# Performance work log

Measured on AMD Instinct MI355X. Metric: run time of the kernel, lower is better.

Reference implementation:

```python
import jax, jax.numpy as jnp
import numpy as np

B, C, H, W = 2, 14, 128, 128
LOSS_WEIGHT = 0.5  # output = (1 - loss_weight) * sum of per-(bs,cls) log-Hausdorff losses
BIG = 1e6          # 'infinite' 1D distance for columns with no background pixel


def _edt_sq(is_zero):
    """Exact squared Euclidean distance transform of a [H,W] bool map.

    Returns, for every pixel, the squared distance to the nearest True pixel
    of `is_zero` (0 at True pixels). Matches scipy.ndimage.distance_transform_edt
    squared. Two-phase separable brute force (vectorized, no data loops).
    """
    h, w = is_zero.shape
    ii = jnp.arange(h, dtype=jnp.float32)
    absd = jnp.abs(ii[:, None] - ii[None, :])  # [H(i), H(p)] = |i - p|
    # d1[i, q] = min_{p : is_zero[p, q]} |i - p|   (per-column 1D distance)
    d1 = jnp.min(jnp.where(is_zero[None, :, :], absd[:, :, None], BIG), axis=1)  # [H, W]
    jj = jnp.arange(w, dtype=jnp.float32)
    off = (jj[:, None] - jj[None, :]) ** 2  # [W(q), W(j)] = (q - j)^2
    # sq[i, j] = min_q d1[i, q]^2 + (q - j)^2
    return jnp.min(d1[:, :, None] ** 2 + off[None, :, :], axis=1)  # [H, W]


def _distance_field_sq(img):
    """MONAI HausdorffDTLoss.distance_field squared: (edt(fg)+edt(bg))^2.

    fg_dist and bg_dist have disjoint supports, so (fg+bg)^2 = fg^2 + bg^2.
    Zero field if the image is all-foreground or all-background.
    """
    fg = img > 0.5
    field = _edt_sq(~fg) + _edt_sq(fg)
    valid = jnp.any(fg) & jnp.any(~fg)
    return jnp.where(valid, field, 0.0)


def _edge_mask(m):
    """mask XOR binary_erosion(mask): scipy default cross structuring element,
    border_value=0 (borders erode)."""
    p = jnp.pad(m, 1, constant_values=False)
    er = m & p[:-2, 1:-1] & p[2:, 1:-1] & p[1:-1, :-2] & p[1:-1, 2:]
    return m & ~er


def _pair_loss(stud_logit, seg_s, seg_t, teach_pred):
    # stud_logit: [H,W] float logits of this class; seg_s/seg_t: [H,W] bool
    # class masks; teach_pred: [H,W] teacher argmax labels (int)
    es = _edge_mask(seg_s).astype(stud_logit.dtype)
    et = _edge_mask(seg_t)
    pred = es * stud_logit                                      # edges * logits
    targ = jnp.where(et, teach_pred.astype(stud_logit.dtype), 0.0)  # edges * labels
    pred_dt2 = jax.lax.stop_gradient(_distance_field_sq(pred))  # MONAI detaches dt
    targ_dt2 = jax.lax.stop_gradient(_distance_field_sq(targ))
    hd = jnp.mean((pred - targ) ** 2 * (pred_dt2 + targ_dt2))   # alpha = 2
    return jnp.log(hd + 1.0)                                    # LogHausdorffDTLoss


def reference(logits_student, logits_teacher):
    ps = jnp.argmax(logits_student, axis=1)  # softmax is monotone -> argmax of logits
    pt = jnp.argmax(logits_teacher, axis=1)
    cls = jnp.arange(1, C)                   # classes 1..C-1 (background skipped)
    n = B * (C - 1)
    seg_s = (ps[:, None] == cls[None, :, None, None]).reshape(n, H, W)
    seg_t = (pt[:, None] == cls[None, :, None, None]).reshape(n, H, W)
    stud = logits_student[:, 1:].reshape(n, H, W)
    pt_rep = jnp.broadcast_to(pt[:, None], (B, C - 1, H, W)).reshape(n, H, W)
    losses = jax.vmap(_pair_loss)(stud, seg_s, seg_t, pt_rep)
    return (1.0 - LOSS_WEIGHT) * jnp.sum(losses)


def setup_inputs() -> dict:
    key = jax.random.key(0)
    k1, k2 = jax.random.split(key)
    return {
        "logits_student": jax.random.normal(k1, (B, C, H, W), dtype=jnp.float32),
        "logits_teacher": jax.random.normal(k2, (B, C, H, W), dtype=jnp.float32),
    }
```

## Files before the change

### kernel.cpp

```cpp
#include <hip/hip_runtime.h>
#include <math.h>
#include <limits.h>

#define HH 128
#define WW 128
#define HW (HH*WW)
#define BB 2
#define CC 14
#define NPAIR 26
#define RPB 8
#define NBLK (NPAIR * (HH / RPB))

typedef unsigned long long u64;


__device__ inline int nbd(u64 lo, u64 hi, int i) {
    int up = 255, down = 255;
    u64 slo, shi;
    if (i == 0)      { slo = lo; shi = hi; }
    else if (i < 64) { slo = (lo >> i) | (hi << (64 - i)); shi = hi >> i; }
    else             { slo = hi >> (i - 64); shi = 0ULL; }
    if (slo)      up = __builtin_ctzll(slo);
    else if (shi) up = 64 + __builtin_ctzll(shi);
    int s = 127 - i;
    u64 llo, lhi;
    if (s == 0)      { llo = lo; lhi = hi; }
    else if (s < 64) { lhi = (hi << s) | (lo >> (64 - s)); llo = lo << s; }
    else             { lhi = lo << (s - 64); llo = 0ULL; }
    if (lhi)      down = __builtin_clzll(lhi);
    else if (llo) down = 64 + __builtin_clzll(llo);
    return min(up, down);
}

__device__ inline ulonglong2 ld16z(const unsigned char* p, size_t off, bool ok) {
    return ok ? *(const ulonglong2*)(p + off) : make_ulonglong2(0ULL, 0ULL);
}

__global__ void k_pack(const float* __restrict__ Ls, const float* __restrict__ Lt,
                       unsigned char* __restrict__ Scol, unsigned char* __restrict__ Tcol,
                       unsigned char* __restrict__ Hcol) {
    int tid = threadIdx.x;
    int p4 = blockIdx.x * 256 + tid;
    int b = p4 >> 12;
    int q4 = p4 & (HW / 4 - 1);
    const float4* bs = (const float4*)(Ls + (size_t)b * CC * HW) + q4;
    const float4* bt = (const float4*)(Lt + (size_t)b * CC * HW) + q4;
    float4 mS = bs[0], mT = bt[0];
    uchar4 iS = make_uchar4(0, 0, 0, 0), iT = make_uchar4(0, 0, 0, 0);
    ushort4 hm = make_ushort4(0, 0, 0, 0);
#pragma unroll
    for (int c = 1; c < CC; ++c) {
        float4 v = bs[(size_t)c * (HW / 4)];
        if (v.x > mS.x) { mS.x = v.x; iS.x = (unsigned char)c; }
        if (v.y > mS.y) { mS.y = v.y; iS.y = (unsigned char)c; }
        if (v.z > mS.z) { mS.z = v.z; iS.z = (unsigned char)c; }
        if (v.w > mS.w) { mS.w = v.w; iS.w = (unsigned char)c; }
        unsigned short bit = (unsigned short)(1u << (c - 1));
        if (v.x > 0.5f) hm.x |= bit;
        if (v.y > 0.5f) hm.y |= bit;
        if (v.z > 0.5f) hm.z |= bit;
        if (v.w > 0.5f) hm.w |= bit;
        float4 u = bt[(size_t)c * (HW / 4)];
        if (u.x > mT.x) { mT.x = u.x; iT.x = (unsigned char)c; }
        if (u.y > mT.y) { mT.y = u.y; iT.y = (unsigned char)c; }
        if (u.z > mT.z) { mT.z = u.z; iT.z = (unsigned char)c; }
        if (u.w > mT.w) { mT.w = u.w; iT.w = (unsigned char)c; }
    }
    __shared__ unsigned char  labL[8][WW];
    __shared__ unsigned short hL[8][WW];
    int r  = tid >> 5;
    int c4 = (tid & 31) * 4;
    *(uchar4*)&labL[r][c4] = make_uchar4(
        (unsigned char)(iS.x | (iT.x << 4)), (unsigned char)(iS.y | (iT.y << 4)),
        (unsigned char)(iS.z | (iT.z << 4)), (unsigned char)(iS.w | (iT.w << 4)));
    *(ushort4*)&hL[r][c4] = hm;
    __syncthreads();

    int j  = tid & (WW - 1);
    int g  = blockIdx.x & 15;
    int n0 = b * CC;
    if (tid < 128) {
        unsigned char lr[8];
#pragma unroll
        for (int rr = 0; rr < 8; ++rr) lr[rr] = labL[rr][j];
#pragma unroll
        for (int cc = 1; cc < CC; ++cc) {
            unsigned int sb = 0, tb = 0;
#pragma unroll
            for (int rr = 0; rr < 8; ++rr) {
                sb |= (unsigned int)((lr[rr] & 15) == cc) << rr;
                tb |= (unsigned int)((lr[rr] >> 4)  == cc) << rr;
            }
            size_t off = ((size_t)(((n0 + cc) << 7) | j) << 4) + g;
            Scol[off] = (unsigned char)sb;
            Tcol[off] = (unsigned char)tb;
        }
    } else {
        unsigned short hr[8];
#pragma unroll
        for (int rr = 0; rr < 8; ++rr) hr[rr] = hL[rr][j];
#pragma unroll
        for (int cc = 1; cc < CC; ++cc) {
            unsigned int hbb = 0;
#pragma unroll
            for (int rr = 0; rr < 8; ++rr) hbb |= ((hr[rr] >> (cc - 1)) & 1u) << rr;
            size_t off = ((size_t)(((n0 + cc) << 7) | j) << 4) + g;
            Hcol[off] = (unsigned char)hbb;
        }
    }
}

__global__ __launch_bounds__(1024) void k_C(
        const unsigned char* __restrict__ Scol, const unsigned char* __restrict__ Tcol,
        const unsigned char* __restrict__ Hcol, const float* __restrict__ Ls,
        float* __restrict__ partials) {
    int n = blockIdx.x >> 4;
    int t = blockIdx.x & 15;
    int tid = threadIdx.x;
    int k = tid >> 7;
    int j = tid & (WW - 1);
    int b = n / (CC - 1), c = 1 + (n - b * (CC - 1));
    const float* Lp = Ls + (size_t)(b * CC + c) * HW;

    int i = t * RPB + k;
    float lv = Lp[i * WW + j];

    __shared__ ulonglong2 colFP[WW], colET[WW], colES[WW];
    __shared__ int sfl[4];

    size_t cbase = ((size_t)(((b * CC + c) << 7) | j)) << 4;
    if (tid < 128) {
        ulonglong2 S  = *(const ulonglong2*)(Scol + cbase);
        ulonglong2 Sl = ld16z(Scol, cbase - 16, j > 0);
        ulonglong2 Sr = ld16z(Scol, cbase + 16, j < WW - 1);
        ulonglong2 Hc = *(const ulonglong2*)(Hcol + cbase);
        u64 ms0 = S.x, ms1 = S.y;
        u64 U0 = ms0 << 1, U1 = (ms1 << 1) | (ms0 >> 63);
        u64 D0 = (ms0 >> 1) | (ms1 << 63), D1 = ms1 >> 1;
        u64 er0 = ms0 & U0 & D0 & Sl.x & Sr.x;
        u64 er1 = ms1 & U1 & D1 & Sl.y & Sr.y;
        u64 es0 = ms0 & ~er0, es1 = ms1 & ~er1;
        u64 fp0 = es0 & Hc.x, fp1 = es1 & Hc.y;
        colES[j] = make_ulonglong2(es0, es1);
        colFP[j] = make_ulonglong2(fp0, fp1);
        u64 bFgP = __ballot((fp0 | fp1) != 0ull);
        u64 bBgP = __ballot((fp0 & fp1) != ~0ull);
        if ((tid & 63) == 0) sfl[tid >> 6] = (bFgP ? 1 : 0) | (bBgP ? 2 : 0);
    } else if (tid < 256) {
        ulonglong2 T  = *(const ulonglong2*)(Tcol + cbase);
        ulonglong2 Tl = ld16z(Tcol, cbase - 16, j > 0);
        ulonglong2 Tr = ld16z(Tcol, cbase + 16, j < WW - 1);
        u64 mt0 = T.x, mt1 = T.y;
        u64 Ut0 = mt0 << 1, Ut1 = (mt1 << 1) | (mt0 >> 63);
        u64 Dt0 = (mt0 >> 1) | (mt1 << 63), Dt1 = mt1 >> 1;
        u64 ert0 = mt0 & Ut0 & Dt0 & Tl.x & Tr.x;
        u64 ert1 = mt1 & Ut1 & Dt1 & Tl.y & Tr.y;
        u64 et0 = mt0 & ~ert0, et1 = mt1 & ~ert1;
        colET[j] = make_ulonglong2(et0, et1);
        u64 bFgT = __ballot((et0 | et1) != 0ull);
        u64 bBgT = __ballot((et0 & et1) != ~0ull);
        if ((tid & 63) == 0) sfl[tid >> 6] = (bFgT ? 4 : 0) | (bBgT ? 8 : 0);
    }
    __syncthreads();

    ulonglong2 mP = colFP[j];
    ulonglong2 mT = colET[j];
    ulonglong2 eS = colES[j];
    int f = sfl[0] | sfl[1] | sfl[2] | sfl[3];
    bool aP = (f & 3) == 3, aT = (f & 12) == 12;

    int dP  = nbd(mP.x, mP.y, i);
    int dPb = nbd(~mP.x, ~mP.y, i);
    int dT  = nbd(mT.x, mT.y, i);
    int dTb = nbd(~mT.x, ~mT.y, i);

    __shared__ uchar4 sq[RPB][WW];
    sq[k][j] = make_uchar4((unsigned char)dP, (unsigned char)dPb,
                           (unsigned char)dT, (unsigned char)dTb);
    __syncthreads();

    int bP = dP * dP, bPb = dPb * dPb, bT = dT * dT, bTb = dTb * dTb;
    int need = 0;
    if (aP) need = max(bP, bPb);
    if (aT) need = max(need, max(bT, bTb));
    for (int rad = 1; rad < WW; ++rad) {
        int rr = rad * rad;
        if (rr >= need) break;
        if (j >= rad) {
            uchar4 s = sq[k][j - rad];
            bP  = min(bP,  (int)s.x * s.x + rr); bPb = min(bPb, (int)s.y * s.y + rr);
            bT  = min(bT,  (int)s.z * s.z + rr); bTb = min(bTb, (int)s.w * s.w + rr);
        }
        if (j + rad < WW) {
            uchar4 s = sq[k][j + rad];
            bP  = min(bP,  (int)s.x * s.x + rr); bPb = min(bPb, (int)s.y * s.y + rr);
            bT  = min(bT,  (int)s.z * s.z + rr); bTb = min(bTb, (int)s.w * s.w + rr);
        }
        need = 0;
        if (aP) need = max(bP, bPb);
        if (aT) need = max(need, max(bT, bTb));
    }

    float fieldP = aP ? (float)(bP + bPb) : 0.0f;
    float fieldT = aT ? (float)(bT + bTb) : 0.0f;

    bool es = ((i < 64 ? (eS.x >> i) : (eS.y >> (i - 64))) & 1ull) != 0;
    bool et = ((i < 64 ? (mT.x >> i) : (mT.y >> (i - 64))) & 1ull) != 0;
    float predv = es ? lv : 0.0f;
    float targv = et ? (float)c : 0.0f;
    float diff = predv - targv;
    float v = diff * diff * (fieldP + fieldT);

    for (int o = 32; o > 0; o >>= 1) v += __shfl_down(v, o);
    __shared__ float wsum[16];
    int lane = tid & 63, w = tid >> 6;
    if (lane == 0) wsum[w] = v;
    __syncthreads();
    if (tid == 0) {
        float tot = 0.0f;
#pragma unroll
        for (int q = 0; q < 16; ++q) tot += wsum[q];
        partials[blockIdx.x] = tot;
    }
}

__global__ void k_fin(const float* __restrict__ partials, float* __restrict__ out) {
    int tid = threadIdx.x;
    float vv = 0.0f;
    if (tid < NPAIR) {
        float s = 0.0f;
#pragma unroll
        for (int t = 0; t < 16; ++t) s += partials[tid * 16 + t];
        vv = logf(s * (1.0f / (float)HW) + 1.0f);
    }
    for (int o = 32; o > 0; o >>= 1) vv += __shfl_down(vv, o);
    if (tid == 0) out[0] = 0.5f * vv;
}

extern "C" void kernel_launch(void* const* d_in, const int* in_sizes, int n_in,
                              void* d_out, int out_size, void* d_ws, size_t ws_size,
                              hipStream_t stream) {
    const float* Ls = (const float*)d_in[0];
    const float* Lt = (const float*)d_in[1];
    float* out = (float*)d_out;

    char* w = (char*)d_ws;
    unsigned char* Sc   = (unsigned char*)(w);
    unsigned char* Tc   = (unsigned char*)(w + 57344);
    unsigned char* Hc   = (unsigned char*)(w + 114688);
    float*         part = (float*)        (w + 172032);

    k_pack<<<BB * HW / 4 / 256, 256, 0, stream>>>(Ls, Lt, Sc, Tc, Hc);
    k_C<<<NBLK, 1024, 0, stream>>>(Sc, Tc, Hc, Ls, part);
    k_fin<<<1, 64, 0, stream>>>(part, out);
}
```

Baseline: 68.60 us.

## Process two rows per thread and compute column masks redundantly per thread

```diff
diff --git a/kernel.cpp b/kernel.cpp
--- a/kernel.cpp
+++ b/kernel.cpp
@@ -8,7 +8,7 @@
 #define BB 2
 #define CC 14
 #define NPAIR 26
-#define RPB 8
+#define RPB 16
 #define NBLK (NPAIR * (HH / RPB))
 
 typedef unsigned long long u64;
@@ -114,102 +114,112 @@
         const unsigned char* __restrict__ Scol, const unsigned char* __restrict__ Tcol,
         const unsigned char* __restrict__ Hcol, const float* __restrict__ Ls,
         float* __restrict__ partials) {
-    int n = blockIdx.x >> 4;
-    int t = blockIdx.x & 15;
+    int n = blockIdx.x >> 3;
+    int g = blockIdx.x & 7;
     int tid = threadIdx.x;
     int k = tid >> 7;
     int j = tid & (WW - 1);
     int b = n / (CC - 1), c = 1 + (n - b * (CC - 1));
     const float* Lp = Ls + (size_t)(b * CC + c) * HW;
 
-    int i = t * RPB + k;
-    float lv = Lp[i * WW + j];
-
-    __shared__ ulonglong2 colFP[WW], colET[WW], colES[WW];
-    __shared__ int sfl[4];
+    int i0 = g * RPB + k;
+    int i1 = i0 + 8;
+    float lv0 = Lp[i0 * WW + j];
+    float lv1 = Lp[i1 * WW + j];
 
     size_t cbase = ((size_t)(((b * CC + c) << 7) | j)) << 4;
+    ulonglong2 S  = *(const ulonglong2*)(Scol + cbase);
+    ulonglong2 Sl = ld16z(Scol, cbase - 16, j > 0);
+    ulonglong2 Sr = ld16z(Scol, cbase + 16, j < WW - 1);
+    ulonglong2 T  = *(const ulonglong2*)(Tcol + cbase);
+    ulonglong2 Tl = ld16z(Tcol, cbase - 16, j > 0);
+    ulonglong2 Tr = ld16z(Tcol, cbase + 16, j < WW - 1);
+    ulonglong2 Hc = *(const ulonglong2*)(Hcol + cbase);
+
+    u64 ms0 = S.x, ms1 = S.y;
+    u64 U0 = ms0 << 1, U1 = (ms1 << 1) | (ms0 >> 63);
+    u64 D0 = (ms0 >> 1) | (ms1 << 63), D1 = ms1 >> 1;
+    u64 er0 = ms0 & U0 & D0 & Sl.x & Sr.x;
+    u64 er1 = ms1 & U1 & D1 & Sl.y & Sr.y;
+    u64 es0 = ms0 & ~er0, es1 = ms1 & ~er1;
+    u64 fp0 = es0 & Hc.x, fp1 = es1 & Hc.y;
+
+    u64 mt0 = T.x, mt1 = T.y;
+    u64 Ut0 = mt0 << 1, Ut1 = (mt1 << 1) | (mt0 >> 63);
+    u64 Dt0 = (mt0 >> 1) | (mt1 << 63), Dt1 = mt1 >> 1;
+    u64 ert0 = mt0 & Ut0 & Dt0 & Tl.x & Tr.x;
+    u64 ert1 = mt1 & Ut1 & Dt1 & Tl.y & Tr.y;
+    u64 et0 = mt0 & ~ert0, et1 = mt1 & ~ert1;
+
+    __shared__ int sfl[2];
+    __shared__ uchar4 sq[RPB][WW];
+
     if (tid < 128) {
-        ulonglong2 S  = *(const ulonglong2*)(Scol + cbase);
-        ulonglong2 Sl = ld16z(Scol, cbase - 16, j > 0);
-        ulonglong2 Sr = ld16z(Scol, cbase + 16, j < WW - 1);
-        ulonglong2 Hc = *(const ulonglong2*)(Hcol + cbase);
-        u64 ms0 = S.x, ms1 = S.y;
-        u64 U0 = ms0 << 1, U1 = (ms1 << 1) | (ms0 >> 63);
-        u64 D0 = (ms0 >> 1) | (ms1 << 63), D1 = ms1 >> 1;
-        u64 er0 = ms0 & U0 & D0 & Sl.x & Sr.x;
-        u64 er1 = ms1 & U1 & D1 & Sl.y & Sr.y;
-        u64 es0 = ms0 & ~er0, es1 = ms1 & ~er1;
-        u64 fp0 = es0 & Hc.x, fp1 = es1 & Hc.y;
-        colES[j] = make_ulonglong2(es0, es1);
-        colFP[j] = make_ulonglong2(fp0, fp1);
         u64 bFgP = __ballot((fp0 | fp1) != 0ull);
         u64 bBgP = __ballot((fp0 & fp1) != ~0ull);
-        if ((tid & 63) == 0) sfl[tid >> 6] = (bFgP ? 1 : 0) | (bBgP ? 2 : 0);
-    } else if (tid < 256) {
-        ulonglong2 T  = *(const ulonglong2*)(Tcol + cbase);
-        ulonglong2 Tl = ld16z(Tcol, cbase - 16, j > 0);
-        ulonglong2 Tr = ld16z(Tcol, cbase + 16, j < WW - 1);
-        u64 mt0 = T.x, mt1 = T.y;
-        u64 Ut0 = mt0 << 1, Ut1 = (mt1 << 1) | (mt0 >> 63);
-        u64 Dt0 = (mt0 >> 1) | (mt1 << 63), Dt1 = mt1 >> 1;
-        u64 ert0 = mt0 & Ut0 & Dt0 & Tl.x & Tr.x;
-        u64 ert1 = mt1 & Ut1 & Dt1 & Tl.y & Tr.y;
-        u64 et0 = mt0 & ~ert0, et1 = mt1 & ~ert1;
-        colET[j] = make_ulonglong2(et0, et1);
         u64 bFgT = __ballot((et0 | et1) != 0ull);
         u64 bBgT = __ballot((et0 & et1) != ~0ull);
-        if ((tid & 63) == 0) sfl[tid >> 6] = (bFgT ? 4 : 0) | (bBgT ? 8 : 0);
-    }
+        if ((tid & 63) == 0)
+            sfl[tid >> 6] = (bFgP ? 1 : 0) | (bBgP ? 2 : 0)
+                          | (bFgT ? 4 : 0) | (bBgT ? 8 : 0);
+    }
+
+    int dP0  = nbd(fp0, fp1, i0),  dPb0 = nbd(~fp0, ~fp1, i0);
+    int dT0  = nbd(et0, et1, i0),  dTb0 = nbd(~et0, ~et1, i0);
+    int dP1  = nbd(fp0, fp1, i1),  dPb1 = nbd(~fp0, ~fp1, i1);
+    int dT1  = nbd(et0, et1, i1),  dTb1 = nbd(~et0, ~et1, i1);
+
+    sq[k][j]     = make_uchar4((unsigned char)dP0, (unsigned char)dPb0,
+                               (unsigned char)dT0, (unsigned char)dTb0);
+    sq[k + 8][j] = make_uchar4((unsigned char)dP1, (unsigned char)dPb1,
+                               (unsigned char)dT1, (unsigned char)dTb1);
     __syncthreads();
 
-    ulonglong2 mP = colFP[j];
-    ulonglong2 mT = colET[j];
-    ulonglong2 eS = colES[j];
-    int f = sfl[0] | sfl[1] | sfl[2] | sfl[3];
+    int f = sfl[0] | sfl[1];
     bool aP = (f & 3) == 3, aT = (f & 12) == 12;
 
-    int dP  = nbd(mP.x, mP.y, i);
-    int dPb = nbd(~mP.x, ~mP.y, i);
-    int dT  = nbd(mT.x, mT.y, i);
-    int dTb = nbd(~mT.x, ~mT.y, i);
-
-    __shared__ uchar4 sq[RPB][WW];
-    sq[k][j] = make_uchar4((unsigned char)dP, (unsigned char)dPb,
-                           (unsigned char)dT, (unsigned char)dTb);
-    __syncthreads();
-
-    int bP = dP * dP, bPb = dPb * dPb, bT = dT * dT, bTb = dTb * dTb;
+    int bP0 = dP0 * dP0, bPb0 = dPb0 * dPb0, bT0 = dT0 * dT0, bTb0 = dTb0 * dTb0;
+    int bP1 = dP1 * dP1, bPb1 = dPb1 * dPb1, bT1 = dT1 * dT1, bTb1 = dTb1 * dTb1;
     int need = 0;
-    if (aP) need = max(bP, bPb);
-    if (aT) need = max(need, max(bT, bTb));
+    if (aP) need = max(max(bP0, bPb0), max(bP1, bPb1));
+    if (aT) need = max(need, max(max(bT0, bTb0), max(bT1, bTb1)));
     for (int rad = 1; rad < WW; ++rad) {
         int rr = rad * rad;
         if (rr >= need) break;
         if (j >= rad) {
-            uchar4 s = sq[k][j - rad];
-            bP  = min(bP,  (int)s.x * s.x + rr); bPb = min(bPb, (int)s.y * s.y + rr);
-            bT  = min(bT,  (int)s.z * s.z + rr); bTb = min(bTb, (int)s.w * s.w + rr);
+            uchar4 sA = sq[k][j - rad];
+            uchar4 sB = sq[k + 8][j - rad];
+            bP0 = min(bP0, (int)sA.x * sA.x + rr); bPb0 = min(bPb0, (int)sA.y * sA.y + rr);
+            bT0 = min(bT0, (int)sA.z * sA.z + rr); bTb0 = min(bTb0, (int)sA.w * sA.w + rr);
+            bP1 = min(bP1, (int)sB.x * sB.x + rr); bPb1 = min(bPb1, (int)sB.y * sB.y + rr);
+            bT1 = min(bT1, (int)sB.z * sB.z + rr); bTb1 = min(bTb1, (int)sB.w * sB.w + rr);
         }
         if (j + rad < WW) {
-            uchar4 s = sq[k][j + rad];
-            bP  = min(bP,  (int)s.x * s.x + rr); bPb = min(bPb, (int)s.y * s.y + rr);
-            bT  = min(bT,  (int)s.z * s.z + rr); bTb = min(bTb, (int)s.w * s.w + rr);
+            uchar4 sA = sq[k][j + rad];
+            uchar4 sB = sq[k + 8][j + rad];
+            bP0 = min(bP0, (int)sA.x * sA.x + rr); bPb0 = min(bPb0, (int)sA.y * sA.y + rr);
+            bT0 = min(bT0, (int)sA.z * sA.z + rr); bTb0 = min(bTb0, (int)sA.w * sA.w + rr);
+            bP1 = min(bP1, (int)sB.x * sB.x + rr); bPb1 = min(bPb1, (int)sB.y * sB.y + rr);
+            bT1 = min(bT1, (int)sB.z * sB.z + rr); bTb1 = min(bTb1, (int)sB.w * sB.w + rr);
         }
         need = 0;
-        if (aP) need = max(bP, bPb);
-        if (aT) need = max(need, max(bT, bTb));
-    }
-
-    float fieldP = aP ? (float)(bP + bPb) : 0.0f;
-    float fieldT = aT ? (float)(bT + bTb) : 0.0f;
-
-    bool es = ((i < 64 ? (eS.x >> i) : (eS.y >> (i - 64))) & 1ull) != 0;
-    bool et = ((i < 64 ? (mT.x >> i) : (mT.y >> (i - 64))) & 1ull) != 0;
-    float predv = es ? lv : 0.0f;
-    float targv = et ? (float)c : 0.0f;
-    float diff = predv - targv;
-    float v = diff * diff * (fieldP + fieldT);
+        if (aP) need = max(max(bP0, bPb0), max(bP1, bPb1));
+        if (aT) need = max(need, max(max(bT0, bTb0), max(bT1, bTb1)));
+    }
+
+    float fieldP0 = aP ? (float)(bP0 + bPb0) : 0.0f;
+    float fieldT0 = aT ? (float)(bT0 + bTb0) : 0.0f;
+    float fieldP1 = aP ? (float)(bP1 + bPb1) : 0.0f;
+    float fieldT1 = aT ? (float)(bT1 + bTb1) : 0.0f;
+
+    bool es_0 = ((i0 < 64 ? (es0 >> i0) : (es1 >> (i0 - 64))) & 1ull) != 0;
+    bool et_0 = ((i0 < 64 ? (et0 >> i0) : (et1 >> (i0 - 64))) & 1ull) != 0;
+    bool es_1 = ((i1 < 64 ? (es0 >> i1) : (es1 >> (i1 - 64))) & 1ull) != 0;
+    bool et_1 = ((i1 < 64 ? (et0 >> i1) : (et1 >> (i1 - 64))) & 1ull) != 0;
+    float pv0 = es_0 ? lv0 : 0.0f, tv0 = et_0 ? (float)c : 0.0f;
+    float pv1 = es_1 ? lv1 : 0.0f, tv1 = et_1 ? (float)c : 0.0f;
+    float d0 = pv0 - tv0, d1 = pv1 - tv1;
+    float v = d0 * d0 * (fieldP0 + fieldT0) + d1 * d1 * (fieldP1 + fieldT1);
 
     for (int o = 32; o > 0; o >>= 1) v += __shfl_down(v, o);
     __shared__ float wsum[16];
@@ -230,7 +240,7 @@
     if (tid < NPAIR) {
         float s = 0.0f;
 #pragma unroll
-        for (int t = 0; t < 16; ++t) s += partials[tid * 16 + t];
+        for (int t = 0; t < 8; ++t) s += partials[tid * 8 + t];
         vv = logf(s * (1.0f / (float)HW) + 1.0f);
     }
     for (int o = 32; o > 0; o >>= 1) vv += __shfl_down(vv, o);
```

Measured after the change: 70.66 us. 3.0% more time.

## Fuse final reduction into main kernel via atomics and widen pack kernel grid

Applied to the files above, without the earlier changes.

```diff
diff --git a/kernel.cpp b/kernel.cpp
--- a/kernel.cpp
+++ b/kernel.cpp
@@ -36,84 +36,72 @@
     return ok ? *(const ulonglong2*)(p + off) : make_ulonglong2(0ULL, 0ULL);
 }
 
-__global__ void k_pack(const float* __restrict__ Ls, const float* __restrict__ Lt,
-                       unsigned char* __restrict__ Scol, unsigned char* __restrict__ Tcol,
-                       unsigned char* __restrict__ Hcol) {
+__global__ __launch_bounds__(256) void k_pack(
+        const float* __restrict__ Ls, const float* __restrict__ Lt,
+        unsigned char* __restrict__ Scol, unsigned char* __restrict__ Tcol,
+        unsigned char* __restrict__ Hcol,
+        float* __restrict__ sums, unsigned int* __restrict__ cnt,
+        float* __restrict__ acc, unsigned int* __restrict__ cnt2) {
     int tid = threadIdx.x;
-    int p4 = blockIdx.x * 256 + tid;
-    int b = p4 >> 12;
-    int q4 = p4 & (HW / 4 - 1);
-    const float4* bs = (const float4*)(Ls + (size_t)b * CC * HW) + q4;
-    const float4* bt = (const float4*)(Lt + (size_t)b * CC * HW) + q4;
-    float4 mS = bs[0], mT = bt[0];
-    uchar4 iS = make_uchar4(0, 0, 0, 0), iT = make_uchar4(0, 0, 0, 0);
-    ushort4 hm = make_ushort4(0, 0, 0, 0);
+    if (blockIdx.x == 0) {
+        if (tid < NPAIR) { sums[tid] = 0.0f; cnt[tid] = 0u; }
+        if (tid == 64)   { *acc = 0.0f; *cnt2 = 0u; }
+    }
+    int blk = blockIdx.x;
+    int b = blk >> 6;
+    int g = (blk >> 2) & 15;
+    int s = blk & 3;
+    int r  = tid >> 5;
+    int jl = tid & 31;
+    int row = g * 8 + r;
+    const float* ps = Ls + (size_t)b * CC * HW + row * WW + s * 32 + jl;
+    const float* pt = Lt + (size_t)b * CC * HW + row * WW + s * 32 + jl;
+    float mS = ps[0], mT = pt[0];
+    int iS = 0, iT = 0;
+    unsigned int hm = 0;
 #pragma unroll
     for (int c = 1; c < CC; ++c) {
-        float4 v = bs[(size_t)c * (HW / 4)];
-        if (v.x > mS.x) { mS.x = v.x; iS.x = (unsigned char)c; }
-        if (v.y > mS.y) { mS.y = v.y; iS.y = (unsigned char)c; }
-        if (v.z > mS.z) { mS.z = v.z; iS.z = (unsigned char)c; }
-        if (v.w > mS.w) { mS.w = v.w; iS.w = (unsigned char)c; }
-        unsigned short bit = (unsigned short)(1u << (c - 1));
-        if (v.x > 0.5f) hm.x |= bit;
-        if (v.y > 0.5f) hm.y |= bit;
-        if (v.z > 0.5f) hm.z |= bit;
-        if (v.w > 0.5f) hm.w |= bit;
-        float4 u = bt[(size_t)c * (HW / 4)];
-        if (u.x > mT.x) { mT.x = u.x; iT.x = (unsigned char)c; }
-        if (u.y > mT.y) { mT.y = u.y; iT.y = (unsigned char)c; }
-        if (u.z > mT.z) { mT.z = u.z; iT.z = (unsigned char)c; }
-        if (u.w > mT.w) { mT.w = u.w; iT.w = (unsigned char)c; }
-    }
-    __shared__ unsigned char  labL[8][WW];
-    __shared__ unsigned short hL[8][WW];
-    int r  = tid >> 5;
-    int c4 = (tid & 31) * 4;
-    *(uchar4*)&labL[r][c4] = make_uchar4(
-        (unsigned char)(iS.x | (iT.x << 4)), (unsigned char)(iS.y | (iT.y << 4)),
-        (unsigned char)(iS.z | (iT.z << 4)), (unsigned char)(iS.w | (iT.w << 4)));
-    *(ushort4*)&hL[r][c4] = hm;
-    __syncthreads();
-
-    int j  = tid & (WW - 1);
-    int g  = blockIdx.x & 15;
+        float v = ps[(size_t)c * HW];
+        if (v > mS) { mS = v; iS = c; }
+        if (v > 0.5f) hm |= 1u << (c - 1);
+        float u = pt[(size_t)c * HW];
+        if (u > mT) { mT = u; iT = c; }
+    }
+    __shared__ unsigned char  labL[8][32];
+    __shared__ unsigned short hL[8][32];
+    labL[r][jl] = (unsigned char)(iS | (iT << 4));
+    hL[r][jl]   = (unsigned short)hm;
+    __syncthreads();
+
+    int jc = tid & 31;
+    int c0 = 1 + (tid >> 5);
+    unsigned char  lr[8];
+    unsigned short hr[8];
+#pragma unroll
+    for (int rr = 0; rr < 8; ++rr) { lr[rr] = labL[rr][jc]; hr[rr] = hL[rr][jc]; }
     int n0 = b * CC;
-    if (tid < 128) {
-        unsigned char lr[8];
-#pragma unroll
-        for (int rr = 0; rr < 8; ++rr) lr[rr] = labL[rr][j];
-#pragma unroll
-        for (int cc = 1; cc < CC; ++cc) {
-            unsigned int sb = 0, tb = 0;
-#pragma unroll
-            for (int rr = 0; rr < 8; ++rr) {
-                sb |= (unsigned int)((lr[rr] & 15) == cc) << rr;
-                tb |= (unsigned int)((lr[rr] >> 4)  == cc) << rr;
-            }
-            size_t off = ((size_t)(((n0 + cc) << 7) | j) << 4) + g;
-            Scol[off] = (unsigned char)sb;
-            Tcol[off] = (unsigned char)tb;
-        }
-    } else {
-        unsigned short hr[8];
-#pragma unroll
-        for (int rr = 0; rr < 8; ++rr) hr[rr] = hL[rr][j];
-#pragma unroll
-        for (int cc = 1; cc < CC; ++cc) {
-            unsigned int hbb = 0;
-#pragma unroll
-            for (int rr = 0; rr < 8; ++rr) hbb |= ((hr[rr] >> (cc - 1)) & 1u) << rr;
-            size_t off = ((size_t)(((n0 + cc) << 7) | j) << 4) + g;
-            Hcol[off] = (unsigned char)hbb;
-        }
+    int jj = s * 32 + jc;
+    for (int cc = c0; cc < CC; cc += 8) {
+        unsigned int sb = 0, tb = 0, hbb = 0;
+#pragma unroll
+        for (int rr = 0; rr < 8; ++rr) {
+            sb  |= (unsigned int)((lr[rr] & 15) == cc) << rr;
+            tb  |= (unsigned int)((lr[rr] >> 4)  == cc) << rr;
+            hbb |= ((unsigned int)(hr[rr] >> (cc - 1)) & 1u) << rr;
+        }
+        size_t off = ((size_t)(((n0 + cc) << 7) | jj) << 4) + g;
+        Scol[off] = (unsigned char)sb;
+        Tcol[off] = (unsigned char)tb;
+        Hcol[off] = (unsigned char)hbb;
     }
 }
 
 __global__ __launch_bounds__(1024) void k_C(
         const unsigned char* __restrict__ Scol, const unsigned char* __restrict__ Tcol,
         const unsigned char* __restrict__ Hcol, const float* __restrict__ Ls,
-        float* __restrict__ partials) {
+        float* __restrict__ sums, unsigned int* __restrict__ cnt,
+        float* __restrict__ acc, unsigned int* __restrict__ cnt2,
+        float* __restrict__ out) {
     int n = blockIdx.x >> 4;
     int t = blockIdx.x & 15;
     int tid = threadIdx.x;
@@ -220,21 +208,25 @@
         float tot = 0.0f;
 #pragma unroll
         for (int q = 0; q < 16; ++q) tot += wsum[q];
-        partials[blockIdx.x] = tot;
-    }
-}
-
-__global__ void k_fin(const float* __restrict__ partials, float* __restrict__ out) {
-    int tid = threadIdx.x;
-    float vv = 0.0f;
-    if (tid < NPAIR) {
-        float s = 0.0f;
-#pragma unroll
-        for (int t = 0; t < 16; ++t) s += partials[tid * 16 + t];
-        vv = logf(s * (1.0f / (float)HW) + 1.0f);
-    }
-    for (int o = 32; o > 0; o >>= 1) vv += __shfl_down(vv, o);
-    if (tid == 0) out[0] = 0.5f * vv;
+        __hip_atomic_fetch_add(&sums[n], tot, __ATOMIC_RELEASE,
+                               __HIP_MEMORY_SCOPE_AGENT);
+        unsigned int prev = __hip_atomic_fetch_add(&cnt[n], 1u, __ATOMIC_ACQ_REL,
+                                                   __HIP_MEMORY_SCOPE_AGENT);
+        if (prev == 15u) {
+            float hd = __hip_atomic_load(&sums[n], __ATOMIC_ACQUIRE,
+                                         __HIP_MEMORY_SCOPE_AGENT)
+                       * (1.0f / (float)HW);
+            float lg = logf(hd + 1.0f);
+            __hip_atomic_fetch_add(acc, lg, __ATOMIC_RELEASE,
+                                   __HIP_MEMORY_SCOPE_AGENT);
+            unsigned int p2 = __hip_atomic_fetch_add(cnt2, 1u, __ATOMIC_ACQ_REL,
+                                                     __HIP_MEMORY_SCOPE_AGENT);
+            if (p2 == NPAIR - 1u) {
+                out[0] = 0.5f * __hip_atomic_load(acc, __ATOMIC_ACQUIRE,
+                                                  __HIP_MEMORY_SCOPE_AGENT);
+            }
+        }
+    }
 }
 
 extern "C" void kernel_launch(void* const* d_in, const int* in_sizes, int n_in,
@@ -248,9 +240,11 @@
     unsigned char* Sc   = (unsigned char*)(w);
     unsigned char* Tc   = (unsigned char*)(w + 57344);
     unsigned char* Hc   = (unsigned char*)(w + 114688);
-    float*         part = (float*)        (w + 172032);
-
-    k_pack<<<BB * HW / 4 / 256, 256, 0, stream>>>(Ls, Lt, Sc, Tc, Hc);
-    k_C<<<NBLK, 1024, 0, stream>>>(Sc, Tc, Hc, Ls, part);
-    k_fin<<<1, 64, 0, stream>>>(part, out);
-}
+    float*         sums = (float*)        (w + 172032);
+    unsigned int*  cnt  = (unsigned int*) (w + 172160);
+    float*         acc  = (float*)        (w + 172288);
+    unsigned int*  cnt2 = (unsigned int*) (w + 172292);
+
+    k_pack<<<BB * 64, 256, 0, stream>>>(Ls, Lt, Sc, Tc, Hc, sums, cnt, acc, cnt2);
+    k_C<<<NBLK, 1024, 0, stream>>>(Sc, Tc, Hc, Ls, sums, cnt, acc, cnt2, out);
+}
```

New measurement: 73.49 us. +7.1%, slower.
